# Kernel optimization log

Hardware: AMD Instinct MI355X
Metric: run time of the kernel (lower is better)

Reference implementation:

```python
import jax, jax.numpy as jnp
import numpy as np

N_NODES = 100000
N_GRAPHS = 64
EPS = 1e-5


def _sage_conv(x, src, dst, Wl, bl, Wr):
    # mean-aggregate neighbor messages (src -> dst), then lin_l(agg) + lin_r(x)
    n = x.shape[0]
    deg = jax.ops.segment_sum(jnp.ones_like(dst, dtype=x.dtype), dst, num_segments=n)
    agg = jax.ops.segment_sum(x[src], dst, num_segments=n)  # [N, d]
    agg = agg / jnp.maximum(deg, 1.0)[:, None]
    return agg @ Wl + bl + x @ Wr


def _bn_relu(x, gamma, beta):
    mu = jnp.mean(x, axis=0)
    var = jnp.var(x, axis=0)
    return jax.nn.relu((x - mu) * jax.lax.rsqrt(var + EPS) * gamma + beta)


def setup_inputs() -> dict:
    key = jax.random.key(0)
    ks = jax.random.split(key, 16)
    E = 1600000
    x = jax.random.normal(ks[0], (N_NODES, 2), dtype=jnp.float32)
    edge_index = jax.random.randint(ks[1], (2, E), 0, N_NODES, dtype=jnp.int64)
    batch = jnp.sort(jax.random.randint(ks[2], (N_NODES,), 0, N_GRAPHS, dtype=jnp.int64))

    def lin(k, din, dout):
        s = 1.0 / np.sqrt(din)
        return jax.random.uniform(k, (din, dout), jnp.float32, -s, s)

    d = {"x": x, "edge_index": edge_index, "batch": batch}
    dims = [(2, 32), (32, 64), (64, 128)]
    for i, (din, dout) in enumerate(dims, 1):
        k1, k2 = jax.random.split(ks[2 + i])
        d[f"Wl{i}"] = lin(k1, din, dout)
        d[f"bl{i}"] = jnp.zeros((dout,), jnp.float32)
        d[f"Wr{i}"] = lin(k2, din, dout)
        d[f"g{i}"] = jnp.ones((dout,), jnp.float32)
        d[f"be{i}"] = jnp.zeros((dout,), jnp.float32)
    d["Wf1"] = lin(ks[10], 128, 64)
    d["bf1"] = jnp.zeros((64,), jnp.float32)
    d["Wf2"] = lin(ks[11], 64, 1)
    d["bf2"] = jnp.zeros((1,), jnp.float32)
    return d


def reference(x, edge_index, batch,
              Wl1, bl1, Wr1, g1, be1,
              Wl2, bl2, Wr2, g2, be2,
              Wl3, bl3, Wr3, g3, be3,
              Wf1, bf1, Wf2, bf2):
    src, dst = edge_index[0], edge_index[1]
    h = _bn_relu(_sage_conv(x, src, dst, Wl1, bl1, Wr1), g1, be1)
    h = _bn_relu(_sage_conv(h, src, dst, Wl2, bl2, Wr2), g2, be2)
    h = _bn_relu(_sage_conv(h, src, dst, Wl3, bl3, Wr3), g3, be3)
    # global mean pool over graphs
    cnt = jax.ops.segment_sum(jnp.ones_like(batch, dtype=h.dtype), batch, num_segments=N_GRAPHS)
    pooled = jax.ops.segment_sum(h, batch, num_segments=N_GRAPHS) / jnp.maximum(cnt, 1.0)[:, None]
    out = jax.nn.relu(pooled @ Wf1 + bf1)
    # dropout is identity in eval mode
    return out @ Wf2 + bf2
```

## Files before the change

kernel.cpp:

```cpp
#include <hip/hip_runtime.h>
#include <hip/hip_fp16.h>

#define N_NODES 100000
#define N_GRAPHS 64
#define BN_EPS 1e-5

#define NB 782
#define NC 49
#define PT1 4096
#define PT2 2048
#define BPC 16
#define CAP 3072

typedef _Float16 f16x8 __attribute__((ext_vector_type(8)));
typedef float f32x4 __attribute__((ext_vector_type(4)));

union F16x8u {
    f16x8 v;
    __half2 h2[4];
    uint4 u;
};

__device__ __forceinline__ float bfly64(float v) {
#pragma unroll
    for (int m = 1; m < 64; m <<= 1) v += __shfl_xor(v, m, 64);
    return v;
}

__device__ __forceinline__ unsigned pack_h2(float a, float b) {
    __half2 h = __floats2half2_rn(a, b);
    unsigned w;
    __builtin_memcpy(&w, &h, 4);
    return w;
}

__device__ __forceinline__ float2 unpack_h2(unsigned w) {
    __half2 h;
    __builtin_memcpy(&h, &w, 4);
    return __half22float2(h);
}

__global__ void hist_fine(const int* __restrict__ dst, int* __restrict__ bhist, int E) {
    __shared__ int h[NB];
    for (int i = threadIdx.x; i < NB; i += 256) h[i] = 0;
    __syncthreads();
    int stride = gridDim.x * 256;
    for (int e = blockIdx.x * 256 + threadIdx.x; e < E; e += stride) {
        int d = __builtin_nontemporal_load(dst + e);
        atomicAdd(&h[d >> 7], 1);
    }
    __syncthreads();
    for (int i = threadIdx.x; i < NB; i += 256)
        if (h[i]) atomicAdd(&bhist[i], h[i]);
}

__global__ void scan_buckets(const int* __restrict__ bhist, int* __restrict__ bo,
                             int* __restrict__ fcur, int* __restrict__ co,
                             int* __restrict__ ccur) {
    __shared__ int sh[1024];
    int t = threadIdx.x;
    sh[t] = (t < NB) ? bhist[t] : 0;
    __syncthreads();
    for (int st = 1; st < 1024; st <<= 1) {
        int v = (t >= st) ? sh[t - st] : 0;
        __syncthreads();
        sh[t] += v;
        __syncthreads();
    }
    int total = sh[NB - 1];
    if (t < NB) {
        int e = t ? sh[t - 1] : 0;
        bo[t] = e; fcur[t] = e;
    } else if (t < 784) {
        if (t == NB) bo[NB] = total;
        fcur[t] = total;
    }
    if (t < NC) {
        int i = t << 4;
        int e = i ? sh[i - 1] : 0;
        co[t] = e; ccur[t] = e;
    } else if (t == NC) {
        co[NC] = total;
    }
}

__global__ __launch_bounds__(256)
void part1(const int* __restrict__ dst, const int* __restrict__ src,
           int* __restrict__ ccur, int* __restrict__ cdst, int* __restrict__ csrc, int E) {
    __shared__ int ld[PT1], ls[PT1];
    __shared__ unsigned char lb[PT1];
    __shared__ int hist[NC], lbase[NC], gbase[NC];
    long long t0 = (long long)blockIdx.x * PT1;
    int n = (int)min((long long)PT1, (long long)E - t0);
    int tid = threadIdx.x;
    for (int i = tid; i < NC; i += 256) hist[i] = 0;
    __syncthreads();
    int d[PT1 / 256], s[PT1 / 256], c[PT1 / 256];
#pragma unroll
    for (int k = 0; k < PT1 / 256; ++k) {
        int li = k * 256 + tid;
        if (li < n) {
            d[k] = __builtin_nontemporal_load(dst + t0 + li);
            s[k] = __builtin_nontemporal_load(src + t0 + li);
            c[k] = d[k] >> 11;
            atomicAdd(&hist[c[k]], 1);
        }
    }
    __syncthreads();
    if (tid == 0) {
        int run = 0;
        for (int i = 0; i < NC; ++i) { lbase[i] = run; run += hist[i]; }
    }
    __syncthreads();
    if (tid < NC) gbase[tid] = atomicAdd(&ccur[tid], hist[tid]);
    __syncthreads();
    for (int i = tid; i < NC; i += 256) hist[i] = 0;
    __syncthreads();
#pragma unroll
    for (int k = 0; k < PT1 / 256; ++k) {
        int li = k * 256 + tid;
        if (li < n) {
            int pos = lbase[c[k]] + atomicAdd(&hist[c[k]], 1);
            ld[pos] = d[k]; ls[pos] = s[k]; lb[pos] = (unsigned char)c[k];
        }
    }
    __syncthreads();
    for (int i = tid; i < n; i += 256) {
        int bb = lb[i];
        int g = gbase[bb] + (i - lbase[bb]);
        cdst[g] = ld[i];
        csrc[g] = ls[i];
    }
}

__global__ __launch_bounds__(256)
void part2(const int* __restrict__ cdst, const int* __restrict__ csrc,
           const int* __restrict__ co, int* __restrict__ fcur,
           int* __restrict__ qdst, int* __restrict__ qsrc) {
    __shared__ int ld[PT2], ls[PT2];
    __shared__ unsigned char lb[PT2];
    __shared__ int hist[16], lbase[16], gbase[16];
    int c = blockIdx.x / BPC;
    int j = blockIdx.x % BPC;
    int beg = co[c], end = co[c + 1];
    int tid = threadIdx.x;
    for (int t0 = beg + j * PT2; t0 < end; t0 += BPC * PT2) {
        int n = min(PT2, end - t0);
        if (tid < 16) hist[tid] = 0;
        __syncthreads();
        int d[PT2 / 256], s[PT2 / 256], f[PT2 / 256];
#pragma unroll
        for (int k = 0; k < PT2 / 256; ++k) {
            int li = k * 256 + tid;
            if (li < n) {
                d[k] = cdst[t0 + li];
                s[k] = csrc[t0 + li];
                f[k] = (d[k] >> 7) & 15;
                atomicAdd(&hist[f[k]], 1);
            }
        }
        __syncthreads();
        if (tid == 0) {
            int run = 0;
            for (int i = 0; i < 16; ++i) { lbase[i] = run; run += hist[i]; }
        }
        __syncthreads();
        if (tid < 16) gbase[tid] = atomicAdd(&fcur[(c << 4) + tid], hist[tid]);
        __syncthreads();
        if (tid < 16) hist[tid] = 0;
        __syncthreads();
#pragma unroll
        for (int k = 0; k < PT2 / 256; ++k) {
            int li = k * 256 + tid;
            if (li < n) {
                int pos = lbase[f[k]] + atomicAdd(&hist[f[k]], 1);
                ld[pos] = d[k]; ls[pos] = s[k]; lb[pos] = (unsigned char)f[k];
            }
        }
        __syncthreads();
        for (int i = tid; i < n; i += 256) {
            int bb = lb[i];
            int g = gbase[bb] + (i - lbase[bb]);
            qdst[g] = ld[i];
            qsrc[g] = ls[i];
        }
        __syncthreads();
    }
}

__global__ __launch_bounds__(256)
void fill_final(const int* __restrict__ qdst, const int* __restrict__ qsrc,
                const int* __restrict__ bo, int* __restrict__ offs,
                int* __restrict__ nbr, int N, int E) {
    __shared__ int cnt[128], cbase[128], cur[128];
    __shared__ int lout[CAP];
    int b = blockIdx.x;
    int nlo = b << 7;
    int nn = min(128, N - nlo);
    int ebeg = bo[b], ne = bo[b + 1] - ebeg;
    int tid = threadIdx.x;
    if (tid < 128) { cnt[tid] = 0; cur[tid] = 0; }
    __syncthreads();
    for (int i = tid; i < ne; i += 256)
        atomicAdd(&cnt[qdst[ebeg + i] - nlo], 1);
    __syncthreads();
    if (tid < 128) cbase[tid] = cnt[tid];
    __syncthreads();
    for (int st = 1; st < 128; st <<= 1) {
        int v = 0;
        if (tid < 128 && tid >= st) v = cbase[tid - st];
        __syncthreads();
        if (tid < 128 && tid >= st) cbase[tid] += v;
        __syncthreads();
    }
    if (tid < nn)
        offs[nlo + tid] = ebeg + (tid ? cbase[tid - 1] : 0);
    if (b == NB - 1 && tid == 0) offs[N] = E;
    __syncthreads();
    for (int i = tid; i < ne; i += 256) {
        int d = qdst[ebeg + i];
        int s = qsrc[ebeg + i];
        int ln = d - nlo;
        int p = (ln ? cbase[ln - 1] : 0) + atomicAdd(&cur[ln], 1);
        lout[p] = s;
    }
    __syncthreads();
    for (int i = tid; i < ne; i += 256)
        nbr[ebeg + i] = lout[i];
}

__global__ __launch_bounds__(256)
void layer1_fused(const float2* __restrict__ x2,
                  const int* __restrict__ offs, const int* __restrict__ nbr,
                  const float* __restrict__ Wl, const float* __restrict__ bl,
                  const float* __restrict__ Wr,
                  __half* __restrict__ hout16,
                  double* __restrict__ sums, int N) {
    __shared__ float sAr[64];
    int tid = threadIdx.x;
    if (tid < 64) sAr[tid] = 0.f;
    __syncthreads();
    int n = blockIdx.x * 256 + tid;
    bool valid = (n < N);
    int beg = 0, end = 0;
    if (valid) { beg = offs[n]; end = offs[n + 1]; }
    double ax = 0.0, ay = 0.0;
    int j = beg;
    for (; j + 4 <= end; j += 4) {
        int s0 = nbr[j], s1 = nbr[j + 1], s2 = nbr[j + 2], s3 = nbr[j + 3];
        float2 v0 = x2[s0], v1 = x2[s1], v2 = x2[s2], v3 = x2[s3];
        ax += v0.x; ay += v0.y;
        ax += v1.x; ay += v1.y;
        ax += v2.x; ay += v2.y;
        ax += v3.x; ay += v3.y;
    }
    for (; j < end; ++j) {
        float2 v = x2[nbr[j]];
        ax += v.x; ay += v.y;
    }
    float invd = 1.0f / fmaxf((float)(end - beg), 1.0f);
    float a0 = (float)ax * invd, a1 = (float)ay * invd;
    float x0 = 0.f, x1 = 0.f;
    if (valid) {
        float2 xv = x2[n];
        x0 = xv.x; x1 = xv.y;
    }
    float acc[32];
#pragma unroll
    for (int jj = 0; jj < 32; ++jj)
        acc[jj] = bl[jj] + a0 * Wl[jj] + a1 * Wl[32 + jj] + x0 * Wr[jj] + x1 * Wr[32 + jj];
    if (valid) {
        unsigned w[16];
#pragma unroll
        for (int p = 0; p < 16; ++p) w[p] = pack_h2(acc[2*p], acc[2*p+1]);
        uint4* q = (uint4*)(hout16 + (size_t)n * 32);
        q[0] = make_uint4(w[0], w[1], w[2], w[3]);
        q[1] = make_uint4(w[4], w[5], w[6], w[7]);
        q[2] = make_uint4(w[8], w[9], w[10], w[11]);
        q[3] = make_uint4(w[12], w[13], w[14], w[15]);
    }
    int lane = tid & 63;
#pragma unroll
    for (int jj = 0; jj < 32; ++jj) {
        float v = valid ? acc[jj] : 0.f;
        float s = bfly64(v);
        float q = bfly64(v * v);
        if (lane == jj) atomicAdd(&sAr[jj], s);
        if (lane == 32 + jj) atomicAdd(&sAr[32 + jj], q);
    }
    __syncthreads();
    if (tid < 64) atomicAdd(&sums[tid], (double)sAr[tid]);
}

template<int F>
__global__ __launch_bounds__(256)
void bn_apply(const uint4* __restrict__ h, const double* __restrict__ sums,
              const float* __restrict__ gamma, const float* __restrict__ beta,
              uint4* __restrict__ out, int N) {
    __shared__ __align__(16) float lsc[F], lsf[F];
    int tid = threadIdx.x;
    if (tid < F) {
        double mu = sums[tid] / (double)N_NODES;
        double var = sums[F + tid] / (double)N_NODES - mu * mu;
        if (var < 0.0) var = 0.0;
        double sc = (double)gamma[tid] / sqrt(var + BN_EPS);
        lsc[tid] = (float)sc;
        lsf[tid] = (float)((double)beta[tid] - mu * sc);
    }
    __syncthreads();
    constexpr int FV = F / 8;
    int total = N * FV;
    for (int i = blockIdx.x * 256 + tid; i < total; i += gridDim.x * 256) {
        uint4 v = h[i];
        int c4 = (i & (FV - 1)) * 2;
        float4 sca = ((const float4*)lsc)[c4];
        float4 scb = ((const float4*)lsc)[c4 + 1];
        float4 sfa = ((const float4*)lsf)[c4];
        float4 sfb = ((const float4*)lsf)[c4 + 1];
        float2 f0 = unpack_h2(v.x), f1 = unpack_h2(v.y);
        float2 f2 = unpack_h2(v.z), f3 = unpack_h2(v.w);
        uint4 o;
        o.x = pack_h2(fmaxf(f0.x * sca.x + sfa.x, 0.f), fmaxf(f0.y * sca.y + sfa.y, 0.f));
        o.y = pack_h2(fmaxf(f1.x * sca.z + sfa.z, 0.f), fmaxf(f1.y * sca.w + sfa.w, 0.f));
        o.z = pack_h2(fmaxf(f2.x * scb.x + sfb.x, 0.f), fmaxf(f2.y * scb.y + sfb.y, 0.f));
        o.w = pack_h2(fmaxf(f3.x * scb.z + sfb.z, 0.f), fmaxf(f3.y * scb.w + sfb.w, 0.f));
        out[i] = o;
    }
}

__device__ __forceinline__ void accum8_h16(float* acc, uint4 v) {
    float2 f0 = unpack_h2(v.x), f1 = unpack_h2(v.y);
    float2 f2 = unpack_h2(v.z), f3 = unpack_h2(v.w);
    acc[0] += f0.x; acc[1] += f0.y; acc[2] += f1.x; acc[3] += f1.y;
    acc[4] += f2.x; acc[5] += f2.y; acc[6] += f3.x; acc[7] += f3.y;
}

template<int F>
__global__ __launch_bounds__(256)
void agg_sum(const uint4* __restrict__ xb, const int* __restrict__ offs,
             const int* __restrict__ nbr, uint4* __restrict__ aggh, int N) {
    constexpr int FV = F / 8;
    constexpr int NPB = 256 / FV;
    int n = blockIdx.x * NPB + threadIdx.y;
    if (n >= N) return;
    int f = threadIdx.x;
    int beg = offs[n], end = offs[n + 1];
    float a0[8], a1[8];
#pragma unroll
    for (int q = 0; q < 8; ++q) { a0[q] = 0.f; a1[q] = 0.f; }
    int j = beg;
    for (; j + 16 <= end; j += 16) {
        int s[16];
#pragma unroll
        for (int u = 0; u < 16; ++u) s[u] = __builtin_nontemporal_load(nbr + j + u);
        uint4 v[16];
#pragma unroll
        for (int u = 0; u < 16; ++u) v[u] = xb[s[u] * FV + f];
#pragma unroll
        for (int u = 0; u < 16; ++u)
            accum8_h16((u & 1) ? a1 : a0, v[u]);
    }
    if (j + 8 <= end) {
        int s[8];
#pragma unroll
        for (int u = 0; u < 8; ++u) s[u] = __builtin_nontemporal_load(nbr + j + u);
        uint4 v[8];
#pragma unroll
        for (int u = 0; u < 8; ++u) v[u] = xb[s[u] * FV + f];
#pragma unroll
        for (int u = 0; u < 8; ++u)
            accum8_h16((u & 1) ? a1 : a0, v[u]);
        j += 8;
    }
    if (j + 4 <= end) {
        int s[4];
#pragma unroll
        for (int u = 0; u < 4; ++u) s[u] = __builtin_nontemporal_load(nbr + j + u);
        uint4 v[4];
#pragma unroll
        for (int u = 0; u < 4; ++u) v[u] = xb[s[u] * FV + f];
#pragma unroll
        for (int u = 0; u < 4; ++u)
            accum8_h16((u & 1) ? a1 : a0, v[u]);
        j += 4;
    }
    for (; j < end; ++j) {
        uint4 v = xb[__builtin_nontemporal_load(nbr + j) * FV + f];
        accum8_h16(a0, v);
    }
    float invd = 1.0f / fmaxf((float)(end - beg), 1.0f);
    uint4 o;
    o.x = pack_h2((a0[0] + a1[0]) * invd, (a0[1] + a1[1]) * invd);
    o.y = pack_h2((a0[2] + a1[2]) * invd, (a0[3] + a1[3]) * invd);
    o.z = pack_h2((a0[4] + a1[4]) * invd, (a0[5] + a1[5]) * invd);
    o.w = pack_h2((a0[6] + a1[6]) * invd, (a0[7] + a1[7]) * invd);
    aggh[n * FV + f] = o;
}

__global__ __launch_bounds__(256)
void pack_w(const float* __restrict__ Wl2, const float* __restrict__ Wr2,
            const float* __restrict__ Wl3, const float* __restrict__ Wr3,
            __half* __restrict__ pk) {
    int e = blockIdx.x * 256 + threadIdx.x;
    const float* W; int le, DOUT, NCB, base, SZ;
    if (e < 2048)       { W = Wl2; le = e;         DOUT = 64;  NCB = 4; base = 0;     SZ = 2048; }
    else if (e < 4096)  { W = Wr2; le = e - 2048;  DOUT = 64;  NCB = 4; base = 4096;  SZ = 2048; }
    else if (e < 12288) { W = Wl3; le = e - 4096;  DOUT = 128; NCB = 8; base = 8192;  SZ = 8192; }
    else                { W = Wr3; le = e - 12288; DOUT = 128; NCB = 8; base = 24576; SZ = 8192; }
    int i = le & 7;
    int lane = (le >> 3) & 63;
    int cbkb = le >> 9;
    int cb = cbkb % NCB;
    int kb = cbkb / NCB;
    int k = kb * 32 + ((lane >> 4) << 3) + i;
    int col = cb * 16 + (lane & 15);
    float w = W[k * DOUT + col];
    __half h = __float2half(w);
    float lo = w - __half2float(h);
    pk[base + le] = h;
    pk[base + SZ + le] = __float2half(lo);
}

template<int DIN, int DOUT>
__global__ __launch_bounds__(256)
void linear_mfma(const __half* __restrict__ bnx16, const __half* __restrict__ agg16,
                 const __half* __restrict__ wlhi, const __half* __restrict__ wllo,
                 const __half* __restrict__ wrhi, const __half* __restrict__ wrlo,
                 const float* __restrict__ bl,
                 __half* __restrict__ hout16, float* __restrict__ partial, int N) {
    constexpr int KB = DIN / 32;
    constexpr int NCB = DOUT / 16;
    constexpr int MREP = 2;
    constexpr int MB = 4 * MREP * 16;
    __shared__ float blkS[DOUT], blkQ[DOUT];
    int tid = threadIdx.x;
    for (int i = tid; i < DOUT; i += 256) { blkS[i] = 0.f; blkQ[i] = 0.f; }
    __syncthreads();
    int n0 = blockIdx.x * MB;

    int wave = tid >> 6;
    int lane = tid & 63;
    int rlane = lane & 15;
    int kg = lane >> 4;
    int rbase = n0 + wave * (MREP * 16);

    f16x8 aA[MREP][KB], aX[MREP][KB];
#pragma unroll
    for (int m = 0; m < MREP; ++m) {
        int row = rbase + m * 16 + rlane;
        int rowc = min(row, N - 1);
#pragma unroll
        for (int kb = 0; kb < KB; ++kb) {
            int c0 = kb * 32 + kg * 8;
            F16x8u ta, tx;
            ta.u = *(const uint4*)(agg16 + (size_t)rowc * DIN + c0);
            tx.u = *(const uint4*)(bnx16 + (size_t)rowc * DIN + c0);
            aA[m][kb] = ta.v;
            aX[m][kb] = tx.v;
        }
    }

    f32x4 acc[MREP][NCB];
#pragma unroll
    for (int cb = 0; cb < NCB; ++cb) {
        float bv = bl[cb * 16 + rlane];
#pragma unroll
        for (int m = 0; m < MREP; ++m)
            acc[m][cb] = {bv, bv, bv, bv};
    }

#pragma unroll
    for (int cb = 0; cb < NCB; ++cb) {
#pragma unroll
        for (int kb = 0; kb < KB; ++kb) {
            size_t fo = ((size_t)(kb * NCB + cb) * 64 + lane) * 8;
            f16x8 blh = *(const f16x8*)(wlhi + fo);
            f16x8 bll = *(const f16x8*)(wllo + fo);
            f16x8 brh = *(const f16x8*)(wrhi + fo);
            f16x8 brl = *(const f16x8*)(wrlo + fo);
#pragma unroll
            for (int m = 0; m < MREP; ++m) {
                acc[m][cb] = __builtin_amdgcn_mfma_f32_16x16x32_f16(aA[m][kb], blh, acc[m][cb], 0, 0, 0);
                acc[m][cb] = __builtin_amdgcn_mfma_f32_16x16x32_f16(aA[m][kb], bll, acc[m][cb], 0, 0, 0);
                acc[m][cb] = __builtin_amdgcn_mfma_f32_16x16x32_f16(aX[m][kb], brh, acc[m][cb], 0, 0, 0);
                acc[m][cb] = __builtin_amdgcn_mfma_f32_16x16x32_f16(aX[m][kb], brl, acc[m][cb], 0, 0, 0);
            }
        }
    }

#pragma unroll
    for (int m = 0; m < MREP; ++m) {
        int rowb = rbase + m * 16 + kg * 4;
#pragma unroll
        for (int r = 0; r < 4; ++r) {
            int node = rowb + r;
            if (node < N) {
#pragma unroll
                for (int cb = 0; cb < NCB; ++cb)
                    hout16[(size_t)node * DOUT + cb * 16 + rlane] = __float2half(acc[m][cb][r]);
            }
        }
    }

#pragma unroll
    for (int cb = 0; cb < NCB; ++cb) {
        float s = 0.f, q = 0.f;
#pragma unroll
        for (int m = 0; m < MREP; ++m) {
            int rowb = rbase + m * 16 + kg * 4;
#pragma unroll
            for (int r = 0; r < 4; ++r) {
                if (rowb + r < N) {
                    float v = acc[m][cb][r];
                    s += v; q += v * v;
                }
            }
        }
        s += __shfl_xor(s, 16, 64); s += __shfl_xor(s, 32, 64);
        q += __shfl_xor(q, 16, 64); q += __shfl_xor(q, 32, 64);
        if (kg == 0) {
            atomicAdd(&blkS[cb * 16 + rlane], s);
            atomicAdd(&blkQ[cb * 16 + rlane], q);
        }
    }
    __syncthreads();
    float* po = partial + (size_t)blockIdx.x * (2 * DOUT);
    for (int i = tid; i < DOUT; i += 256) {
        po[i] = blkS[i];
        po[DOUT + i] = blkQ[i];
    }
}

template<int F>
__global__ __launch_bounds__(256)
void stats_finalize2(const float* __restrict__ partial, double* __restrict__ sums, int P) {
    __shared__ double sh[256];
    int i = blockIdx.x;
    int t = threadIdx.x;
    double a = 0.0;
    for (int k = t; k < P; k += 256)
        a += (double)partial[(size_t)k * (2 * F) + i];
    sh[t] = a;
    __syncthreads();
    for (int st = 128; st > 0; st >>= 1) {
        if (t < st) sh[t] += sh[t + st];
        __syncthreads();
    }
    if (t == 0) sums[i] = sh[0];
}

__global__ void pool_partial(const __half* __restrict__ h, const int* __restrict__ batch,
                             const double* __restrict__ sums,
                             const float* __restrict__ gamma, const float* __restrict__ beta,
                             double* __restrict__ pooled_d, int N) {
    __shared__ float lsc[128], lsf[128];
    const int CH = 64;
    int f = threadIdx.x;
    {
        double mu = sums[f] / (double)N_NODES;
        double var = sums[128 + f] / (double)N_NODES - mu * mu;
        if (var < 0.0) var = 0.0;
        double sc = (double)gamma[f] / sqrt(var + BN_EPS);
        lsc[f] = (float)sc;
        lsf[f] = (float)((double)beta[f] - mu * sc);
    }
    __syncthreads();
    int n0 = blockIdx.x * CH;
    if (n0 >= N) return;
    int n1 = min(n0 + CH, N);
    float sc = lsc[f], sf = lsf[f];
    int g = batch[n0];
    float acc = 0.f;
    for (int n = n0; n < n1; ++n) {
        int bg = batch[n];
        if (bg != g) {
            atomicAdd(&pooled_d[g * 128 + f], (double)acc);
            acc = 0.f;
            g = bg;
        }
        float v = __half2float(h[(long long)n * 128 + f]);
        acc += fmaxf(v * sc + sf, 0.f);
    }
    atomicAdd(&pooled_d[g * 128 + f], (double)acc);
}

__global__ void mlp_fused(const double* __restrict__ pooled_d, const int* __restrict__ batch,
                          const float* __restrict__ Wf1, const float* __restrict__ bf1,
                          const float* __restrict__ Wf2, const float* __restrict__ bf2,
                          float* __restrict__ out, int N) {
    __shared__ float sp[128];
    int g = blockIdx.x;
    int t = threadIdx.x;
    int lo = 0, hi = N;
    while (lo < hi) { int m = (lo + hi) >> 1; if (batch[m] < g) lo = m + 1; else hi = m; }
    int start = lo;
    hi = N;
    while (lo < hi) { int m = (lo + hi) >> 1; if (batch[m] < g + 1) lo = m + 1; else hi = m; }
    int cnt = lo - start;
    sp[t] = (float)(pooled_d[g * 128 + t] / (double)max(cnt, 1));
    __syncthreads();
    if (t < 64) {
        float hacc = bf1[t];
#pragma unroll 8
        for (int k = 0; k < 128; ++k) hacc += sp[k] * Wf1[k * 64 + t];
        hacc = fmaxf(hacc, 0.f) * Wf2[t];
        for (int o = 32; o > 0; o >>= 1) hacc += __shfl_down(hacc, o);
        if (t == 0) out[g] = hacc + bf2[0];
    }
}

extern "C" void kernel_launch(void* const* d_in, const int* in_sizes, int n_in,
                              void* d_out, int out_size, void* d_ws, size_t ws_size,
                              hipStream_t stream) {
    const float* x     = (const float*)d_in[0];
    const int*   ei    = (const int*)d_in[1];
    const int*   batch = (const int*)d_in[2];
    const float *Wl1=(const float*)d_in[3],  *bl1=(const float*)d_in[4],  *Wr1=(const float*)d_in[5];
    const float *g1 =(const float*)d_in[6],  *be1=(const float*)d_in[7];
    const float *Wl2=(const float*)d_in[8],  *bl2=(const float*)d_in[9],  *Wr2=(const float*)d_in[10];
    const float *g2 =(const float*)d_in[11], *be2=(const float*)d_in[12];
    const float *Wl3=(const float*)d_in[13], *bl3=(const float*)d_in[14], *Wr3=(const float*)d_in[15];
    const float *g3 =(const float*)d_in[16], *be3=(const float*)d_in[17];
    const float *Wf1=(const float*)d_in[18], *bf1=(const float*)d_in[19];
    const float *Wf2=(const float*)d_in[20], *bf2=(const float*)d_in[21];

    const int N = N_NODES;
    const int E = in_sizes[1] / 2;
    const int* src = ei;
    const int* dst = ei + E;

    char* ws = (char*)d_ws;
    size_t off = 0;
    auto salloc = [&](size_t bytes) {
        void* p = ws + off;
        off += (bytes + 255) & ~(size_t)255;
        return p;
    };
    int*    bhist   = (int*)   salloc(NB * 4);
    double* sums    = (double*)salloc(768 * 8);
    double* pooledd = (double*)salloc((size_t)N_GRAPHS * 128 * 8);
    size_t zero_bytes = off;
    int*    offs    = (int*)   salloc((size_t)(N + 1) * 4);
    int*    bo      = (int*)   salloc((NB + 1) * 4);
    int*    fcur    = (int*)   salloc(784 * 4);
    int*    co      = (int*)   salloc((NC + 1) * 4);
    int*    ccur    = (int*)   salloc(NC * 4);
    int*    nbr     = (int*)   salloc((size_t)E * 4);
    float*  partial = (float*) salloc((size_t)1024 * 256 * 4);
    __half* pk      = (__half*)salloc((size_t)40960 * 2);
    __half* h1h     = (__half*)salloc((size_t)(N + 256) * 32 * 2);
    __half* b1h     = (__half*)salloc((size_t)(N + 256) * 32 * 2);
    __half* h2h     = (__half*)salloc((size_t)(N + 256) * 64 * 2);
    __half* b2h     = (__half*)salloc((size_t)(N + 256) * 64 * 2);
    __half* h3h     = (__half*)salloc((size_t)(N + 256) * 128 * 2);
    __half* aggh    = (__half*)salloc((size_t)(N + 256) * 64 * 2);
    (void)ws_size;

    double* sums1 = sums, *sums2 = sums + 256, *sums3 = sums + 512;
    int* cdst = (int*)h3h;
    int* csrc = cdst + E;
    int* qdst = (int*)aggh;
    int* qsrc = qdst + E;

    const __half *pwl2h = pk,         *pwl2l = pk + 2048;
    const __half *pwr2h = pk + 4096,  *pwr2l = pk + 6144;
    const __half *pwl3h = pk + 8192,  *pwl3l = pk + 16384;
    const __half *pwr3h = pk + 24576, *pwr3l = pk + 32768;

    hipMemsetAsync(bhist, 0, zero_bytes, stream);

    pack_w<<<80, 256, 0, stream>>>(Wl2, Wr2, Wl3, Wr3, pk);

    hist_fine<<<1024, 256, 0, stream>>>(dst, bhist, E);
    scan_buckets<<<1, 1024, 0, stream>>>(bhist, bo, fcur, co, ccur);
    part1<<<(E + PT1 - 1) / PT1, 256, 0, stream>>>(dst, src, ccur, cdst, csrc, E);
    part2<<<NC * BPC, 256, 0, stream>>>(cdst, csrc, co, fcur, qdst, qsrc);
    fill_final<<<NB, 256, 0, stream>>>(qdst, qsrc, bo, offs, nbr, N, E);

    const int NL = (N + 255) / 256;
    const int NBLK = (N + 127) / 128;

    layer1_fused<<<NL, 256, 0, stream>>>((const float2*)x, offs, nbr,
                                          Wl1, bl1, Wr1, h1h, sums1, N);

    bn_apply<32><<<512, 256, 0, stream>>>((const uint4*)h1h, sums1, g1, be1, (uint4*)b1h, N);
    agg_sum<32><<<(N + 63) / 64, dim3(4, 64), 0, stream>>>(
        (const uint4*)b1h, offs, nbr, (uint4*)aggh, N);
    linear_mfma<32, 64><<<NBLK, 256, 0, stream>>>(
        b1h, (const __half*)aggh, pwl2h, pwl2l, pwr2h, pwr2l, bl2, h2h, partial, N);
    stats_finalize2<64><<<128, 256, 0, stream>>>(partial, sums2, NBLK);

    bn_apply<64><<<512, 256, 0, stream>>>((const uint4*)h2h, sums2, g2, be2, (uint4*)b2h, N);
    agg_sum<64><<<(N + 31) / 32, dim3(8, 32), 0, stream>>>(
        (const uint4*)b2h, offs, nbr, (uint4*)aggh, N);
    linear_mfma<64, 128><<<NBLK, 256, 0, stream>>>(
        b2h, (const __half*)aggh, pwl3h, pwl3l, pwr3h, pwr3l, bl3, h3h, partial, N);
    stats_finalize2<128><<<256, 256, 0, stream>>>(partial, sums3, NBLK);

    pool_partial<<<(N + 63) / 64, 128, 0, stream>>>(h3h, batch, sums3, g3, be3, pooledd, N);
    mlp_fused<<<N_GRAPHS, 128, 0, stream>>>(pooledd, batch, Wf1, bf1, Wf2, bf2, (float*)d_out, N);
}
```

Before: 339.8 us.

## Replace two-pass radix partition CSR build with atomic degree count and scatter

Replaces the bucketed multi-pass partitioning (hist, scan, part1, part2, fill_final) with a per-node degree histogram using global atomics, a three-kernel prefix scan, and an atomic-cursor scatter into the neighbor list. This removes the intermediate bucket copies and shared-memory staging, at the cost of 1.6M contended global atomics and a neighbor order within each node that is no longer deterministic. Layer-1 aggregation also switches from double to two float accumulators with 16-wide unrolled gathers and nontemporal index loads, trading some accumulation precision for more memory-level parallelism.

```diff
diff --git a/kernel.cpp b/kernel.cpp
--- a/kernel.cpp
+++ b/kernel.cpp
@@ -4,13 +4,7 @@
 #define N_NODES 100000
 #define N_GRAPHS 64
 #define BN_EPS 1e-5
-
-#define NB 782
-#define NC 49
-#define PT1 4096
-#define PT2 2048
-#define BPC 16
-#define CAP 3072
+#define NSB 98
 
 typedef _Float16 f16x8 __attribute__((ext_vector_type(8)));
 typedef float f32x4 __attribute__((ext_vector_type(4)));
@@ -40,193 +34,86 @@
     return __half22float2(h);
 }
 
-__global__ void hist_fine(const int* __restrict__ dst, int* __restrict__ bhist, int E) {
-    __shared__ int h[NB];
-    for (int i = threadIdx.x; i < NB; i += 256) h[i] = 0;
-    __syncthreads();
+__global__ __launch_bounds__(256)
+void deg_count(const int* __restrict__ dst, int* __restrict__ deg, int E) {
     int stride = gridDim.x * 256;
     for (int e = blockIdx.x * 256 + threadIdx.x; e < E; e += stride) {
         int d = __builtin_nontemporal_load(dst + e);
-        atomicAdd(&h[d >> 7], 1);
-    }
-    __syncthreads();
-    for (int i = threadIdx.x; i < NB; i += 256)
-        if (h[i]) atomicAdd(&bhist[i], h[i]);
-}
-
-__global__ void scan_buckets(const int* __restrict__ bhist, int* __restrict__ bo,
-                             int* __restrict__ fcur, int* __restrict__ co,
-                             int* __restrict__ ccur) {
-    __shared__ int sh[1024];
+        atomicAdd(&deg[d], 1);
+    }
+}
+
+__global__ __launch_bounds__(256)
+void scan_a(const int* __restrict__ deg, int* __restrict__ bsum, int N) {
+    __shared__ int ws[4];
+    int tid = threadIdx.x;
+    int i0 = blockIdx.x * 1024 + tid * 4;
+    int s = 0;
+    if (i0 < N) {
+        int4 v = *(const int4*)(deg + i0);
+        s = v.x + v.y + v.z + v.w;
+    }
+    for (int m = 1; m < 64; m <<= 1) s += __shfl_xor(s, m, 64);
+    if ((tid & 63) == 0) ws[tid >> 6] = s;
+    __syncthreads();
+    if (tid == 0) bsum[blockIdx.x] = ws[0] + ws[1] + ws[2] + ws[3];
+}
+
+__global__ void scan_b(const int* __restrict__ bsum, int* __restrict__ bbase) {
+    __shared__ int sh[128];
     int t = threadIdx.x;
-    sh[t] = (t < NB) ? bhist[t] : 0;
-    __syncthreads();
-    for (int st = 1; st < 1024; st <<= 1) {
+    sh[t] = (t < NSB) ? bsum[t] : 0;
+    __syncthreads();
+    for (int st = 1; st < 128; st <<= 1) {
         int v = (t >= st) ? sh[t - st] : 0;
         __syncthreads();
         sh[t] += v;
         __syncthreads();
     }
-    int total = sh[NB - 1];
-    if (t < NB) {
-        int e = t ? sh[t - 1] : 0;
-        bo[t] = e; fcur[t] = e;
-    } else if (t < 784) {
-        if (t == NB) bo[NB] = total;
-        fcur[t] = total;
-    }
-    if (t < NC) {
-        int i = t << 4;
-        int e = i ? sh[i - 1] : 0;
-        co[t] = e; ccur[t] = e;
-    } else if (t == NC) {
-        co[NC] = total;
-    }
-}
-
-__global__ __launch_bounds__(256)
-void part1(const int* __restrict__ dst, const int* __restrict__ src,
-           int* __restrict__ ccur, int* __restrict__ cdst, int* __restrict__ csrc, int E) {
-    __shared__ int ld[PT1], ls[PT1];
-    __shared__ unsigned char lb[PT1];
-    __shared__ int hist[NC], lbase[NC], gbase[NC];
-    long long t0 = (long long)blockIdx.x * PT1;
-    int n = (int)min((long long)PT1, (long long)E - t0);
+    if (t < NSB) bbase[t] = t ? sh[t - 1] : 0;
+}
+
+__global__ __launch_bounds__(256)
+void scan_c(const int* __restrict__ deg, const int* __restrict__ bbase,
+            int* __restrict__ offs, int* __restrict__ cur, int N, int E) {
+    __shared__ int sh[256];
     int tid = threadIdx.x;
-    for (int i = tid; i < NC; i += 256) hist[i] = 0;
-    __syncthreads();
-    int d[PT1 / 256], s[PT1 / 256], c[PT1 / 256];
-#pragma unroll
-    for (int k = 0; k < PT1 / 256; ++k) {
-        int li = k * 256 + tid;
-        if (li < n) {
-            d[k] = __builtin_nontemporal_load(dst + t0 + li);
-            s[k] = __builtin_nontemporal_load(src + t0 + li);
-            c[k] = d[k] >> 11;
-            atomicAdd(&hist[c[k]], 1);
-        }
-    }
-    __syncthreads();
-    if (tid == 0) {
-        int run = 0;
-        for (int i = 0; i < NC; ++i) { lbase[i] = run; run += hist[i]; }
-    }
-    __syncthreads();
-    if (tid < NC) gbase[tid] = atomicAdd(&ccur[tid], hist[tid]);
-    __syncthreads();
-    for (int i = tid; i < NC; i += 256) hist[i] = 0;
-    __syncthreads();
-#pragma unroll
-    for (int k = 0; k < PT1 / 256; ++k) {
-        int li = k * 256 + tid;
-        if (li < n) {
-            int pos = lbase[c[k]] + atomicAdd(&hist[c[k]], 1);
-            ld[pos] = d[k]; ls[pos] = s[k]; lb[pos] = (unsigned char)c[k];
-        }
-    }
-    __syncthreads();
-    for (int i = tid; i < n; i += 256) {
-        int bb = lb[i];
-        int g = gbase[bb] + (i - lbase[bb]);
-        cdst[g] = ld[i];
-        csrc[g] = ls[i];
-    }
-}
-
-__global__ __launch_bounds__(256)
-void part2(const int* __restrict__ cdst, const int* __restrict__ csrc,
-           const int* __restrict__ co, int* __restrict__ fcur,
-           int* __restrict__ qdst, int* __restrict__ qsrc) {
-    __shared__ int ld[PT2], ls[PT2];
-    __shared__ unsigned char lb[PT2];
-    __shared__ int hist[16], lbase[16], gbase[16];
-    int c = blockIdx.x / BPC;
-    int j = blockIdx.x % BPC;
-    int beg = co[c], end = co[c + 1];
-    int tid = threadIdx.x;
-    for (int t0 = beg + j * PT2; t0 < end; t0 += BPC * PT2) {
-        int n = min(PT2, end - t0);
-        if (tid < 16) hist[tid] = 0;
+    int i0 = blockIdx.x * 1024 + tid * 4;
+    int d0 = 0, d1 = 0, d2 = 0, d3 = 0;
+    if (i0 < N) {
+        int4 v = *(const int4*)(deg + i0);
+        d0 = v.x; d1 = v.y; d2 = v.z; d3 = v.w;
+    }
+    int t3 = d0 + d1 + d2 + d3;
+    sh[tid] = t3;
+    __syncthreads();
+    for (int st = 1; st < 256; st <<= 1) {
+        int v = (tid >= st) ? sh[tid - st] : 0;
         __syncthreads();
-        int d[PT2 / 256], s[PT2 / 256], f[PT2 / 256];
-#pragma unroll
-        for (int k = 0; k < PT2 / 256; ++k) {
-            int li = k * 256 + tid;
-            if (li < n) {
-                d[k] = cdst[t0 + li];
-                s[k] = csrc[t0 + li];
-                f[k] = (d[k] >> 7) & 15;
-                atomicAdd(&hist[f[k]], 1);
-            }
-        }
+        sh[tid] += v;
         __syncthreads();
-        if (tid == 0) {
-            int run = 0;
-            for (int i = 0; i < 16; ++i) { lbase[i] = run; run += hist[i]; }
-        }
-        __syncthreads();
-        if (tid < 16) gbase[tid] = atomicAdd(&fcur[(c << 4) + tid], hist[tid]);
-        __syncthreads();
-        if (tid < 16) hist[tid] = 0;
-        __syncthreads();
-#pragma unroll
-        for (int k = 0; k < PT2 / 256; ++k) {
-            int li = k * 256 + tid;
-            if (li < n) {
-                int pos = lbase[f[k]] + atomicAdd(&hist[f[k]], 1);
-                ld[pos] = d[k]; ls[pos] = s[k]; lb[pos] = (unsigned char)f[k];
-            }
-        }
-        __syncthreads();
-        for (int i = tid; i < n; i += 256) {
-            int bb = lb[i];
-            int g = gbase[bb] + (i - lbase[bb]);
-            qdst[g] = ld[i];
-            qsrc[g] = ls[i];
-        }
-        __syncthreads();
-    }
-}
-
-__global__ __launch_bounds__(256)
-void fill_final(const int* __restrict__ qdst, const int* __restrict__ qsrc,
-                const int* __restrict__ bo, int* __restrict__ offs,
-                int* __restrict__ nbr, int N, int E) {
-    __shared__ int cnt[128], cbase[128], cur[128];
-    __shared__ int lout[CAP];
-    int b = blockIdx.x;
-    int nlo = b << 7;
-    int nn = min(128, N - nlo);
-    int ebeg = bo[b], ne = bo[b + 1] - ebeg;
-    int tid = threadIdx.x;
-    if (tid < 128) { cnt[tid] = 0; cur[tid] = 0; }
-    __syncthreads();
-    for (int i = tid; i < ne; i += 256)
-        atomicAdd(&cnt[qdst[ebeg + i] - nlo], 1);
-    __syncthreads();
-    if (tid < 128) cbase[tid] = cnt[tid];
-    __syncthreads();
-    for (int st = 1; st < 128; st <<= 1) {
-        int v = 0;
-        if (tid < 128 && tid >= st) v = cbase[tid - st];
-        __syncthreads();
-        if (tid < 128 && tid >= st) cbase[tid] += v;
-        __syncthreads();
-    }
-    if (tid < nn)
-        offs[nlo + tid] = ebeg + (tid ? cbase[tid - 1] : 0);
-    if (b == NB - 1 && tid == 0) offs[N] = E;
-    __syncthreads();
-    for (int i = tid; i < ne; i += 256) {
-        int d = qdst[ebeg + i];
-        int s = qsrc[ebeg + i];
-        int ln = d - nlo;
-        int p = (ln ? cbase[ln - 1] : 0) + atomicAdd(&cur[ln], 1);
-        lout[p] = s;
-    }
-    __syncthreads();
-    for (int i = tid; i < ne; i += 256)
-        nbr[ebeg + i] = lout[i];
+    }
+    int ex = bbase[blockIdx.x] + (tid ? sh[tid - 1] : 0);
+    if (i0 < N) {
+        int4 o;
+        o.x = ex; o.y = ex + d0; o.z = ex + d0 + d1; o.w = ex + d0 + d1 + d2;
+        *(int4*)(offs + i0) = o;
+        *(int4*)(cur + i0) = o;
+        if (i0 + 4 == N) offs[N] = ex + t3;
+    }
+    (void)E;
+}
+
+__global__ __launch_bounds__(256)
+void scatter(const int* __restrict__ dst, const int* __restrict__ src,
+             int* __restrict__ cur, int* __restrict__ nbr, int E) {
+    int stride = gridDim.x * 256;
+    for (int e = blockIdx.x * 256 + threadIdx.x; e < E; e += stride) {
+        int d = __builtin_nontemporal_load(dst + e);
+        int s = __builtin_nontemporal_load(src + e);
+        int p = atomicAdd(&cur[d], 1);
+        nbr[p] = s;
+    }
 }
 
 __global__ __launch_bounds__(256)
@@ -244,22 +131,39 @@
     bool valid = (n < N);
     int beg = 0, end = 0;
     if (valid) { beg = offs[n]; end = offs[n + 1]; }
-    double ax = 0.0, ay = 0.0;
+    float ax0 = 0.f, ay0 = 0.f, ax1 = 0.f, ay1 = 0.f;
     int j = beg;
+    for (; j + 16 <= end; j += 16) {
+        int s[16];
+#pragma unroll
+        for (int u = 0; u < 16; ++u) s[u] = __builtin_nontemporal_load(nbr + j + u);
+        float2 v[16];
+#pragma unroll
+        for (int u = 0; u < 16; ++u) v[u] = x2[s[u]];
+#pragma unroll
+        for (int u = 0; u < 16; ++u) {
+            if (u & 1) { ax1 += v[u].x; ay1 += v[u].y; }
+            else       { ax0 += v[u].x; ay0 += v[u].y; }
+        }
+    }
     for (; j + 4 <= end; j += 4) {
-        int s0 = nbr[j], s1 = nbr[j + 1], s2 = nbr[j + 2], s3 = nbr[j + 3];
-        float2 v0 = x2[s0], v1 = x2[s1], v2 = x2[s2], v3 = x2[s3];
-        ax += v0.x; ay += v0.y;
-        ax += v1.x; ay += v1.y;
-        ax += v2.x; ay += v2.y;
-        ax += v3.x; ay += v3.y;
+        int s[4];
+#pragma unroll
+        for (int u = 0; u < 4; ++u) s[u] = __builtin_nontemporal_load(nbr + j + u);
+        float2 v[4];
+#pragma unroll
+        for (int u = 0; u < 4; ++u) v[u] = x2[s[u]];
+        ax0 += v[0].x; ay0 += v[0].y;
+        ax1 += v[1].x; ay1 += v[1].y;
+        ax0 += v[2].x; ay0 += v[2].y;
+        ax1 += v[3].x; ay1 += v[3].y;
     }
     for (; j < end; ++j) {
         float2 v = x2[nbr[j]];
-        ax += v.x; ay += v.y;
+        ax0 += v.x; ay0 += v.y;
     }
     float invd = 1.0f / fmaxf((float)(end - beg), 1.0f);
-    float a0 = (float)ax * invd, a1 = (float)ay * invd;
+    float a0 = (ax0 + ax1) * invd, a1 = (ay0 + ay1) * invd;
     float x0 = 0.f, x1 = 0.f;
     if (valid) {
         float2 xv = x2[n];
@@ -636,15 +540,14 @@
         off += (bytes + 255) & ~(size_t)255;
         return p;
     };
-    int*    bhist   = (int*)   salloc(NB * 4);
+    int*    deg     = (int*)   salloc((size_t)N * 4);
     double* sums    = (double*)salloc(768 * 8);
     double* pooledd = (double*)salloc((size_t)N_GRAPHS * 128 * 8);
     size_t zero_bytes = off;
-    int*    offs    = (int*)   salloc((size_t)(N + 1) * 4);
-    int*    bo      = (int*)   salloc((NB + 1) * 4);
-    int*    fcur    = (int*)   salloc(784 * 4);
-    int*    co      = (int*)   salloc((NC + 1) * 4);
-    int*    ccur    = (int*)   salloc(NC * 4);
+    int*    offs    = (int*)   salloc((size_t)(N + 4) * 4);
+    int*    cur     = (int*)   salloc((size_t)N * 4);
+    int*    bsum    = (int*)   salloc(128 * 4);
+    int*    bbase   = (int*)   salloc(128 * 4);
     int*    nbr     = (int*)   salloc((size_t)E * 4);
     float*  partial = (float*) salloc((size_t)1024 * 256 * 4);
     __half* pk      = (__half*)salloc((size_t)40960 * 2);
@@ -657,25 +560,21 @@
     (void)ws_size;
 
     double* sums1 = sums, *sums2 = sums + 256, *sums3 = sums + 512;
-    int* cdst = (int*)h3h;
-    int* csrc = cdst + E;
-    int* qdst = (int*)aggh;
-    int* qsrc = qdst + E;
 
     const __half *pwl2h = pk,         *pwl2l = pk + 2048;
     const __half *pwr2h = pk + 4096,  *pwr2l = pk + 6144;
     const __half *pwl3h = pk + 8192,  *pwl3l = pk + 16384;
     const __half *pwr3h = pk + 24576, *pwr3l = pk + 32768;
 
-    hipMemsetAsync(bhist, 0, zero_bytes, stream);
+    hipMemsetAsync(deg, 0, zero_bytes, stream);
 
     pack_w<<<80, 256, 0, stream>>>(Wl2, Wr2, Wl3, Wr3, pk);
 
-    hist_fine<<<1024, 256, 0, stream>>>(dst, bhist, E);
-    scan_buckets<<<1, 1024, 0, stream>>>(bhist, bo, fcur, co, ccur);
-    part1<<<(E + PT1 - 1) / PT1, 256, 0, stream>>>(dst, src, ccur, cdst, csrc, E);
-    part2<<<NC * BPC, 256, 0, stream>>>(cdst, csrc, co, fcur, qdst, qsrc);
-    fill_final<<<NB, 256, 0, stream>>>(qdst, qsrc, bo, offs, nbr, N, E);
+    deg_count<<<1024, 256, 0, stream>>>(dst, deg, E);
+    scan_a<<<NSB, 256, 0, stream>>>(deg, bsum, N);
+    scan_b<<<1, 128, 0, stream>>>(bsum, bbase);
+    scan_c<<<NSB, 256, 0, stream>>>(deg, bbase, offs, cur, N, E);
+    scatter<<<1024, 256, 0, stream>>>(dst, src, cur, nbr, E);
 
     const int NL = (N + 255) / 256;
     const int NBLK = (N + 127) / 128;
```

New measurement: 443.8 us. 1.31x slower.
